# Kernel tuning notes

Measured on AMD Instinct MI355X. Metric: run time of the kernel, lower is better.

The kernel has to match this reference:

```python
import jax, jax.numpy as jnp
import numpy as np

B, S, H = 2, 2048, 2048
NH, NKV, D = 16, 8, 128
THETA = 10000.0
EPS = 1e-6
SCALE = D ** -0.5


def setup_inputs() -> dict:
    key = jax.random.key(0)
    k0, k1, k2 = jax.random.split(key, 3)
    hidden_states = jax.random.normal(k0, (B, S, H), dtype=jnp.float32)
    position_ids = jnp.arange(B * S, dtype=jnp.int64).reshape(B, S) % S
    w_qkv = jax.random.normal(k1, (NH * D + 2 * NKV * D, H), dtype=jnp.float32) * 0.02
    w_o = jax.random.normal(k2, (H, NH * D), dtype=jnp.float32) * 0.02
    q_norm_w = jnp.ones((D,), dtype=jnp.float32)
    k_norm_w = jnp.ones((D,), dtype=jnp.float32)
    return {"hidden_states": hidden_states, "position_ids": position_ids,
            "w_qkv": w_qkv, "w_o": w_o, "q_norm_w": q_norm_w, "k_norm_w": k_norm_w}


def _rms_norm(x, w):
    # x: [..., D]; vLLM RMSNorm: x * rsqrt(mean(x^2) + eps) * w
    var = jnp.mean(x * x, axis=-1, keepdims=True)
    return x * jax.lax.rsqrt(var + EPS) * w


def _rope_gptj(x, positions):
    # non-neox (GPT-J interleaved) RoPE. x: [B, S, nheads, D], positions: [B, S]
    inv_freq = 1.0 / (THETA ** (jnp.arange(0, D, 2, dtype=jnp.float32) / D))  # [D/2]
    freqs = positions.astype(jnp.float32)[..., None] * inv_freq  # [B, S, D/2]
    cos = jnp.repeat(jnp.cos(freqs), 2, axis=-1)[:, :, None, :]  # [B, S, 1, D]
    sin = jnp.repeat(jnp.sin(freqs), 2, axis=-1)[:, :, None, :]
    x1 = x[..., ::2]
    x2 = x[..., 1::2]
    rot = jnp.stack([-x2, x1], axis=-1).reshape(x.shape)  # interleaved rotate
    return x * cos + rot * sin


def reference(hidden_states, position_ids, w_qkv, w_o, q_norm_w, k_norm_w):
    bsz, seq_len, _ = hidden_states.shape
    qkv = jnp.einsum('bsh,oh->bso', hidden_states, w_qkv)  # [B, S, q+2kv]
    q, k, v = jnp.split(qkv, [NH * D, NH * D + NKV * D], axis=-1)
    q = q.reshape(bsz, seq_len, NH, D)
    k = k.reshape(bsz, seq_len, NKV, D)
    v = v.reshape(bsz, seq_len, NKV, D)
    q = _rms_norm(q, q_norm_w)
    k = _rms_norm(k, k_norm_w)
    q = _rope_gptj(q, position_ids)
    k = _rope_gptj(k, position_ids)
    # GQA: group q heads over kv heads
    G = NH // NKV
    qg = q.reshape(bsz, seq_len, NKV, G, D)
    # scores: [B, NKV, G, S, S]
    scores = jnp.einsum('bqhgd,bkhd->bhgqk', qg, k) * SCALE
    causal = jnp.tril(jnp.ones((seq_len, seq_len), dtype=bool))
    scores = jnp.where(causal, scores, jnp.float32(-1e30))
    probs = jax.nn.softmax(scores, axis=-1)
    out = jnp.einsum('bhgqk,bkhd->bqhgd', probs, v)  # [B, S, NKV, G, D]
    out = out.reshape(bsz, seq_len, NH * D)
    return jnp.einsum('bsd,hd->bsh', out, w_o)  # [B, S, H]
```

## Files before the change

### kernel.cpp

```cpp
#include <hip/hip_runtime.h>
#include <hip/hip_bf16.h>
#include <cstdint>
#include <cstddef>


typedef __attribute__((ext_vector_type(8))) short bf16x8;
typedef __attribute__((ext_vector_type(4))) float f32x4;

#define B_ 2
#define S_ 2048
#define H_ 2048
#define NH_ 16
#define NKV_ 8
#define D_ 128
#define BS_ 4096
#define QKVO_ 4096

__device__ __forceinline__ unsigned short f2bf(float f) {
  union { float f; unsigned u; } v; v.f = f;
  unsigned u = v.u;
  u += 0x7fffu + ((u >> 16) & 1u);
  return (unsigned short)(u >> 16);
}

__device__ __forceinline__ void gload_lds16(const void* g, void* l) {
  __builtin_amdgcn_global_load_lds(
      (const __attribute__((address_space(1))) unsigned int*)g,
      (__attribute__((address_space(3))) unsigned int*)l, 16, 0, 0);
}

__global__ void k_f32_to_bf16(const float* __restrict__ x,
                              unsigned short* __restrict__ y, int n4) {
  int i = blockIdx.x * blockDim.x + threadIdx.x;
  if (i >= n4) return;
  float4 v = ((const float4*)x)[i];
  ushort4 o;
  o.x = f2bf(v.x); o.y = f2bf(v.y); o.z = f2bf(v.z); o.w = f2bf(v.w);
  ((ushort4*)y)[i] = o;
}

#define BM 128
#define BN 128
#define BK 32

__global__ __launch_bounds__(256, 2) void k_gemm_bf16(
    const unsigned short* __restrict__ A, const unsigned short* __restrict__ Bm,
    float* __restrict__ C, int M, int N, int K) {
  __shared__ __align__(16) char lds[2][2][BM * BK * 2];

  int nwg = gridDim.x;
  int bid = blockIdx.x;
  int cpx = nwg >> 3;
  int swz = (bid & 7) * cpx + (bid >> 3);
  int nbn = N / BN;
  int bm = swz / nbn, bn = swz % nbn;

  int tid = threadIdx.x;
  int lane = tid & 63, w = tid >> 6;
  int wr = w >> 1, wc = w & 1;
  int lq = lane & 15, lk = lane >> 4;

  const unsigned short* Abase = A + (size_t)bm * BM * K;
  const unsigned short* Bbase = Bm + (size_t)bn * BN * K;

  f32x4 acc[4][4] = {};
  int nt = K / BK;

  auto stage = [&](int buf, int t) {
#pragma unroll
    for (int j = 0; j < 2; ++j) {
      int s = (tid + j * 256) * 16;
      int row = s >> 6;
      int cb = s & 48;
      int cs = cb ^ (((row >> 1) & 3) << 4);
      const char* ga = (const char*)(Abase + (size_t)row * K + t * BK) + cs;
      const char* gb = (const char*)(Bbase + (size_t)row * K + t * BK) + cs;
      gload_lds16(ga, &lds[buf][0][s]);
      gload_lds16(gb, &lds[buf][1][s]);
    }
  };

  stage(0, 0);
  __syncthreads();

  int cur = 0;
  for (int t = 0; t < nt; ++t) {
    if (t + 1 < nt) stage(cur ^ 1, t + 1);
    bf16x8 af[4], bfr[4];
#pragma unroll
    for (int m = 0; m < 4; ++m) {
      int row = wr * 64 + m * 16 + lq;
      int addr = row * 64 + ((lk * 16) ^ (((row >> 1) & 3) << 4));
      af[m] = *(const bf16x8*)(&lds[cur][0][addr]);
    }
#pragma unroll
    for (int n = 0; n < 4; ++n) {
      int row = wc * 64 + n * 16 + lq;
      int addr = row * 64 + ((lk * 16) ^ (((row >> 1) & 3) << 4));
      bfr[n] = *(const bf16x8*)(&lds[cur][1][addr]);
    }
#pragma unroll
    for (int m = 0; m < 4; ++m)
#pragma unroll
      for (int n = 0; n < 4; ++n)
        acc[m][n] = __builtin_amdgcn_mfma_f32_16x16x32_bf16(af[m], bfr[n], acc[m][n], 0, 0, 0);
    __syncthreads();
    cur ^= 1;
  }

#pragma unroll
  for (int m = 0; m < 4; ++m) {
    int row0 = bm * BM + wr * 64 + m * 16 + lk * 4;
#pragma unroll
    for (int n = 0; n < 4; ++n) {
      int col = bn * BN + wc * 64 + n * 16 + lq;
#pragma unroll
      for (int r = 0; r < 4; ++r)
        C[(size_t)(row0 + r) * N + col] = acc[m][n][r];
    }
  }
}

__global__ void k_norm_rope(const float* __restrict__ qkv,
                            const int* __restrict__ pos,
                            const float* __restrict__ qw,
                            const float* __restrict__ kw,
                            unsigned short* __restrict__ Qb,
                            unsigned short* __restrict__ Kb) {
  int g = blockIdx.x * 4 + (threadIdx.x >> 6);
  int lane = threadIdx.x & 63;
  int t = g / 24;
  int slot = g % 24;
  bool isq = slot < 16;
  int h = isq ? slot : slot - 16;
  int off = isq ? h * D_ : NH_ * D_ + h * D_;
  const float* w = isq ? qw : kw;

  float2 x = *(const float2*)(qkv + (size_t)t * QKVO_ + off + lane * 2);
  float ss = x.x * x.x + x.y * x.y;
#pragma unroll
  for (int o = 1; o < 64; o <<= 1) ss += __shfl_xor(ss, o);
  float inv = rsqrtf(ss * (1.0f / 128.0f) + 1e-6f);
  float2 wv = *(const float2*)(w + lane * 2);
  float x1 = x.x * inv * wv.x;
  float x2 = x.y * inv * wv.y;

  float p = (float)pos[t];
  float invf = exp2f(-(float)(lane * 2) * (13.287712379549449f / 128.0f));
  float ang = p * invf;
  float sn, cs;
  sincosf(ang, &sn, &cs);
  float y1 = x1 * cs - x2 * sn;
  float y2 = x2 * cs + x1 * sn;

  int b = t >> 11;
  int sq = t & (S_ - 1);
  size_t o_;
  unsigned short* dst;
  if (isq) { o_ = (((size_t)b * NH_ + h) * S_ + sq) * D_ + lane * 2; dst = Qb; }
  else     { o_ = (((size_t)b * NKV_ + h) * S_ + sq) * D_ + lane * 2; dst = Kb; }
  ushort2 ov; ov.x = f2bf(y1); ov.y = f2bf(y2);
  *(ushort2*)(dst + o_) = ov;
}

__global__ void k_v_transpose(const float* __restrict__ qkv,
                              unsigned short* __restrict__ Vt) {
  __shared__ unsigned short tile[128][72];
  int bidx = blockIdx.x;
  int st = bidx & 31;
  int kh = (bidx >> 5) & 7;
  int b = bidx >> 8;
  int s0 = st * 64;
  int tid = threadIdx.x;
#pragma unroll
  for (int i = 0; i < 8; ++i) {
    int idx = tid + i * 256;
    int row = idx >> 5, c4 = idx & 31;
    float4 v = *(const float4*)(qkv + ((size_t)(b * S_ + s0 + row)) * QKVO_ +
                                (NH_ + NKV_) * D_ + kh * D_ + c4 * 4);
    tile[c4 * 4 + 0][row] = f2bf(v.x);
    tile[c4 * 4 + 1][row] = f2bf(v.y);
    tile[c4 * 4 + 2][row] = f2bf(v.z);
    tile[c4 * 4 + 3][row] = f2bf(v.w);
  }
  __syncthreads();
#pragma unroll
  for (int i = 0; i < 8; ++i) {
    int idx = tid + i * 256;
    int d = idx >> 4, c4 = idx & 15;
    ushort4 o;
    o.x = tile[d][c4 * 4 + 0]; o.y = tile[d][c4 * 4 + 1];
    o.z = tile[d][c4 * 4 + 2]; o.w = tile[d][c4 * 4 + 3];
    *(ushort4*)(Vt + ((((size_t)b * NKV_ + kh) * D_ + d) * S_) + s0 + c4 * 4) = o;
  }
}

#define QBLK 128
#define KVB 64

__global__ __launch_bounds__(256, 2) void k_attn(
    const unsigned short* __restrict__ Qb, const unsigned short* __restrict__ Kb,
    const unsigned short* __restrict__ Vt, unsigned short* __restrict__ Ob) {
  __shared__ __align__(16) char Ks[2][KVB * D_ * 2];
  __shared__ __align__(16) char Vs[2][D_ * KVB * 2];
  __shared__ __align__(16) char Ps[4][32 * KVB * 2];

  int x = blockIdx.x;
  int u = x & 255;
  int hi = x >> 8;
  int k_ = u & 15;
  int qt = hi ? k_ : 15 - k_;
  int h = u >> 4;
  int b = hi;
  int kvh = h >> 1;
  int q0 = qt * QBLK;
  int tid = threadIdx.x, lane = tid & 63, w = tid >> 6;
  int lq = lane & 15, lk = lane >> 4;

  const unsigned short* Qhead = Qb + ((size_t)b * NH_ + h) * S_ * D_;
  const unsigned short* Khead = Kb + ((size_t)b * NKV_ + kvh) * S_ * D_;
  const unsigned short* Vthead = Vt + ((size_t)b * NKV_ + kvh) * D_ * S_;

  bf16x8 qf[2][4];
#pragma unroll
  for (int m = 0; m < 2; ++m)
#pragma unroll
    for (int ks = 0; ks < 4; ++ks)
      qf[m][ks] = *(const bf16x8*)(Qhead +
          (size_t)(q0 + w * 32 + m * 16 + lq) * D_ + ks * 32 + lk * 8);

  f32x4 o_acc[2][8] = {};
  float mrow[2][4], lrow[2][4];
#pragma unroll
  for (int m = 0; m < 2; ++m)
#pragma unroll
    for (int r = 0; r < 4; ++r) { mrow[m][r] = -1e30f; lrow[m][r] = 0.0f; }

  int ntile = q0 / KVB + 2;

  auto stageKV = [&](int buf, int t) {
    int kv0 = t * KVB;
#pragma unroll
    for (int j = 0; j < 4; ++j) {
      int s = (tid + j * 256) * 16;
      {
        int row = s >> 8, cb = s & 255;
        int cs = cb ^ ((row & 7) << 4);
        const char* g = (const char*)(Khead + (size_t)(kv0 + row) * D_) + cs;
        gload_lds16(g, &Ks[buf][s]);
      }
      {
        int row = s >> 7, cb = s & 127;
        int cs = cb ^ ((row & 7) << 4);
        const char* g = (const char*)(Vthead + (size_t)row * S_ + kv0) + cs;
        gload_lds16(g, &Vs[buf][s]);
      }
    }
  };

  stageKV(0, 0);
  __syncthreads();

  const float c1 = 0.08838834764831845f * 1.4426950408889634f;

  int cur = 0;
  for (int t = 0; t < ntile; ++t) {
    if (t + 1 < ntile) stageKV(cur ^ 1, t + 1);
    int kv0 = t * KVB;

    f32x4 sc[2][4] = {};
#pragma unroll
    for (int ks = 0; ks < 4; ++ks) {
      bf16x8 kf[4];
#pragma unroll
      for (int n = 0; n < 4; ++n) {
        int row = n * 16 + lq;
        int addr = row * 256 + ((ks * 64 + lk * 16) ^ ((row & 7) << 4));
        kf[n] = *(const bf16x8*)(&Ks[cur][addr]);
      }
#pragma unroll
      for (int m = 0; m < 2; ++m)
#pragma unroll
        for (int n = 0; n < 4; ++n)
          sc[m][n] = __builtin_amdgcn_mfma_f32_16x16x32_bf16(qf[m][ks], kf[n], sc[m][n], 0, 0, 0);
    }

    bool diag = (kv0 + KVB > q0);
#pragma unroll
    for (int m = 0; m < 2; ++m) {
      float pm[4][4];
      float corr[4];
#pragma unroll
      for (int r = 0; r < 4; ++r) {
        int qg = q0 + w * 32 + m * 16 + lk * 4 + r;
        float vmax = -1e30f;
        float sv[4];
#pragma unroll
        for (int n = 0; n < 4; ++n) {
          float xv = sc[m][n][r] * c1;
          if (diag && (kv0 + n * 16 + lq > qg)) xv = -1e30f;
          sv[n] = xv;
          vmax = fmaxf(vmax, xv);
        }
#pragma unroll
        for (int o = 1; o < 16; o <<= 1) vmax = fmaxf(vmax, __shfl_xor(vmax, o));
        float mnew = fmaxf(mrow[m][r], vmax);
        float cr = exp2f(mrow[m][r] - mnew);
        mrow[m][r] = mnew;
        float rs = 0.0f;
#pragma unroll
        for (int n = 0; n < 4; ++n) {
          float pv = exp2f(sv[n] - mnew);
          pm[n][r] = pv;
          rs += pv;
        }
#pragma unroll
        for (int o = 1; o < 16; o <<= 1) rs += __shfl_xor(rs, o);
        lrow[m][r] = lrow[m][r] * cr + rs;
        corr[r] = cr;
      }
#pragma unroll
      for (int nd = 0; nd < 8; ++nd)
#pragma unroll
        for (int r = 0; r < 4; ++r) o_acc[m][nd][r] *= corr[r];
#pragma unroll
      for (int n = 0; n < 4; ++n)
#pragma unroll
        for (int r = 0; r < 4; ++r) {
          int qlocal = m * 16 + lk * 4 + r;
          int kb = (n * 16 + lq) * 2;
          int addr = qlocal * 128 + (kb ^ ((qlocal & 7) << 4));
          *(unsigned short*)(&Ps[w][addr]) = f2bf(pm[n][r]);
        }
    }

#pragma unroll
    for (int ks = 0; ks < 2; ++ks) {
      bf16x8 pa[2];
#pragma unroll
      for (int m = 0; m < 2; ++m) {
        int row = m * 16 + lq;
        int addr = row * 128 + ((ks * 64 + lk * 16) ^ ((row & 7) << 4));
        pa[m] = *(const bf16x8*)(&Ps[w][addr]);
      }
#pragma unroll
      for (int nd = 0; nd < 8; ++nd) {
        int row = nd * 16 + lq;
        int addr = row * 128 + ((ks * 64 + lk * 16) ^ ((row & 7) << 4));
        bf16x8 vf = *(const bf16x8*)(&Vs[cur][addr]);
#pragma unroll
        for (int m = 0; m < 2; ++m)
          o_acc[m][nd] = __builtin_amdgcn_mfma_f32_16x16x32_bf16(pa[m], vf, o_acc[m][nd], 0, 0, 0);
      }
    }
    __syncthreads();
    cur ^= 1;
  }

#pragma unroll
  for (int m = 0; m < 2; ++m)
#pragma unroll
    for (int r = 0; r < 4; ++r) {
      float rl = 1.0f / lrow[m][r];
      int qg = q0 + w * 32 + m * 16 + lk * 4 + r;
      size_t base = ((size_t)b * S_ + qg) * (NH_ * D_) + h * D_;
#pragma unroll
      for (int nd = 0; nd < 8; ++nd)
        Ob[base + nd * 16 + lq] = f2bf(o_acc[m][nd][r] * rl);
    }
}

extern "C" void kernel_launch(void* const* d_in, const int* in_sizes, int n_in,
                              void* d_out, int out_size, void* d_ws, size_t ws_size,
                              hipStream_t stream) {
  const float* hs    = (const float*)d_in[0];
  const int*   pos   = (const int*)d_in[1];
  const float* w_qkv = (const float*)d_in[2];
  const float* w_o   = (const float*)d_in[3];
  const float* qw    = (const float*)d_in[4];
  const float* kw    = (const float*)d_in[5];
  float* out = (float*)d_out;

  char* ws = (char*)d_ws;
  unsigned short* Xbf  = (unsigned short*)ws;
  unsigned short* Wqbf = Xbf + (size_t)BS_ * H_;
  unsigned short* Wobf = Wqbf + (size_t)QKVO_ * H_;
  float* qkv = (float*)(Wobf + (size_t)H_ * (NH_ * D_));
  unsigned short* Qb  = (unsigned short*)(qkv + (size_t)BS_ * QKVO_);
  unsigned short* Kb  = Qb + (size_t)B_ * NH_ * S_ * D_;
  unsigned short* Vtb = Kb + (size_t)B_ * NKV_ * S_ * D_;
  unsigned short* Ab  = Vtb + (size_t)B_ * NKV_ * S_ * D_;

  k_f32_to_bf16<<<(BS_ * H_ / 4) / 256, 256, 0, stream>>>(hs, Xbf, BS_ * H_ / 4);
  k_f32_to_bf16<<<(QKVO_ * H_ / 4) / 256, 256, 0, stream>>>(w_qkv, Wqbf, QKVO_ * H_ / 4);
  k_f32_to_bf16<<<(H_ * NH_ * D_ / 4) / 256, 256, 0, stream>>>(w_o, Wobf, H_ * NH_ * D_ / 4);

  k_gemm_bf16<<<(BS_ / BM) * (QKVO_ / BN), 256, 0, stream>>>(
      Xbf, Wqbf, qkv, BS_, QKVO_, H_);

  k_norm_rope<<<BS_ * 24 / 4, 256, 0, stream>>>(qkv, pos, qw, kw, Qb, Kb);

  k_v_transpose<<<B_ * NKV_ * (S_ / 64), 256, 0, stream>>>(qkv, Vtb);

  k_attn<<<(S_ / QBLK) * NH_ * B_, 256, 0, stream>>>(Qb, Kb, Vtb, Ab);

  k_gemm_bf16<<<(BS_ / BM) * (H_ / BN), 256, 0, stream>>>(
      Ab, Wobf, out, BS_, H_, H_);
}
```

Baseline: 416.8 us.

## Pair causal query strips per 512-thread block and transpose score MFMA layout

Each attention block now has 8 waves and handles two 128-row query strips, one with a light causal load and one with a heavy one, so work is balanced within a block and only 256 blocks are launched. The waves share K/V staging in LDS, and waves whose strip has finished skip compute while still joining the barriers. The score MFMA operands are swapped so each lane holds one query row, which makes the softmax reductions cheaper (two shuffles instead of four). P is packed with the hardware bf16 pack instruction, and s_setprio is raised around the MFMA sections. In exchange, the light-strip waves sit idle for part of the loop, and the larger blocks may reduce occupancy.

```diff
diff --git a/kernel.cpp b/kernel.cpp
--- a/kernel.cpp
+++ b/kernel.cpp
@@ -21,6 +21,12 @@
   unsigned u = v.u;
   u += 0x7fffu + ((u >> 16) & 1u);
   return (unsigned short)(u >> 16);
+}
+
+__device__ __forceinline__ unsigned cvt_pk_bf16(float lo, float hi) {
+  unsigned r;
+  asm("v_cvt_pk_bf16_f32 %0, %1, %2" : "=v"(r) : "v"(lo), "v"(hi));
+  return r;
 }
 
 __device__ __forceinline__ void gload_lds16(const void* g, void* l) {
@@ -195,27 +201,28 @@
   }
 }
 
-#define QBLK 128
 #define KVB 64
 
-__global__ __launch_bounds__(256, 2) void k_attn(
+__global__ __launch_bounds__(512, 2) void k_attn(
     const unsigned short* __restrict__ Qb, const unsigned short* __restrict__ Kb,
     const unsigned short* __restrict__ Vt, unsigned short* __restrict__ Ob) {
   __shared__ __align__(16) char Ks[2][KVB * D_ * 2];
   __shared__ __align__(16) char Vs[2][D_ * KVB * 2];
-  __shared__ __align__(16) char Ps[4][32 * KVB * 2];
+  __shared__ __align__(16) char Ps[8][32 * KVB * 2];
 
   int x = blockIdx.x;
-  int u = x & 255;
-  int hi = x >> 8;
-  int k_ = u & 15;
-  int qt = hi ? k_ : 15 - k_;
-  int h = u >> 4;
-  int b = hi;
+  int kk = x >> 5;
+  int bh = x & 31;
+  int b = bh >> 4, h = bh & 15;
   int kvh = h >> 1;
-  int q0 = qt * QBLK;
+
   int tid = threadIdx.x, lane = tid & 63, w = tid >> 6;
   int lq = lane & 15, lk = lane >> 4;
+  int strip = w >> 2, wq = w & 3;
+  int qt = strip ? kk : 15 - kk;
+  int q0w = qt * 128 + wq * 32;
+  int nt_w = ((q0w + 31) >> 6) + 1;
+  int nt_max = 2 * (15 - kk) + 2;
 
   const unsigned short* Qhead = Qb + ((size_t)b * NH_ + h) * S_ * D_;
   const unsigned short* Khead = Kb + ((size_t)b * NKV_ + kvh) * S_ * D_;
@@ -227,22 +234,17 @@
 #pragma unroll
     for (int ks = 0; ks < 4; ++ks)
       qf[m][ks] = *(const bf16x8*)(Qhead +
-          (size_t)(q0 + w * 32 + m * 16 + lq) * D_ + ks * 32 + lk * 8);
+          (size_t)(q0w + m * 16 + lq) * D_ + ks * 32 + lk * 8);
 
   f32x4 o_acc[2][8] = {};
-  float mrow[2][4], lrow[2][4];
-#pragma unroll
-  for (int m = 0; m < 2; ++m)
-#pragma unroll
-    for (int r = 0; r < 4; ++r) { mrow[m][r] = -1e30f; lrow[m][r] = 0.0f; }
-
-  int ntile = q0 / KVB + 2;
+  float mrow[2] = {-1e30f, -1e30f};
+  float lrow[2] = {0.0f, 0.0f};
 
   auto stageKV = [&](int buf, int t) {
     int kv0 = t * KVB;
 #pragma unroll
-    for (int j = 0; j < 4; ++j) {
-      int s = (tid + j * 256) * 16;
+    for (int j = 0; j < 2; ++j) {
+      int s = (tid + j * 512) * 16;
       {
         int row = s >> 8, cb = s & 255;
         int cs = cb ^ ((row & 7) << 4);
@@ -250,9 +252,9 @@
         gload_lds16(g, &Ks[buf][s]);
       }
       {
-        int row = s >> 7, cb = s & 127;
-        int cs = cb ^ ((row & 7) << 4);
-        const char* g = (const char*)(Vthead + (size_t)row * S_ + kv0) + cs;
+        int rv = s >> 7, cv = s & 127;
+        int cs = cv ^ ((rv & 7) << 4);
+        const char* g = (const char*)(Vthead + (size_t)rv * S_ + kv0) + cs;
         gload_lds16(g, &Vs[buf][s]);
       }
     }
@@ -264,94 +266,103 @@
   const float c1 = 0.08838834764831845f * 1.4426950408889634f;
 
   int cur = 0;
-  for (int t = 0; t < ntile; ++t) {
-    if (t + 1 < ntile) stageKV(cur ^ 1, t + 1);
-    int kv0 = t * KVB;
-
-    f32x4 sc[2][4] = {};
-#pragma unroll
-    for (int ks = 0; ks < 4; ++ks) {
-      bf16x8 kf[4];
-#pragma unroll
-      for (int n = 0; n < 4; ++n) {
-        int row = n * 16 + lq;
-        int addr = row * 256 + ((ks * 64 + lk * 16) ^ ((row & 7) << 4));
-        kf[n] = *(const bf16x8*)(&Ks[cur][addr]);
+  for (int t = 0; t < nt_max; ++t) {
+    if (t + 1 < nt_max) stageKV(cur ^ 1, t + 1);
+    if (t < nt_w) {
+      int kv0 = t * KVB;
+
+      f32x4 sc[4][2] = {};
+      __builtin_amdgcn_s_setprio(1);
+#pragma unroll
+      for (int ks = 0; ks < 4; ++ks) {
+        bf16x8 kf[4];
+#pragma unroll
+        for (int n = 0; n < 4; ++n) {
+          int row = n * 16 + lq;
+          int addr = row * 256 + ((ks * 64 + lk * 16) ^ ((row & 7) << 4));
+          kf[n] = *(const bf16x8*)(&Ks[cur][addr]);
+        }
+#pragma unroll
+        for (int n = 0; n < 4; ++n)
+#pragma unroll
+          for (int m = 0; m < 2; ++m)
+            sc[n][m] = __builtin_amdgcn_mfma_f32_16x16x32_bf16(kf[n], qf[m][ks], sc[n][m], 0, 0, 0);
       }
-#pragma unroll
-      for (int m = 0; m < 2; ++m)
+      __builtin_amdgcn_s_setprio(0);
+
+      bool diag = (kv0 + KVB > q0w);
+#pragma unroll
+      for (int m = 0; m < 2; ++m) {
+        int qg = q0w + m * 16 + lq;
+        float sv[4][4];
+        float vmax = -1e30f;
 #pragma unroll
         for (int n = 0; n < 4; ++n)
-          sc[m][n] = __builtin_amdgcn_mfma_f32_16x16x32_bf16(qf[m][ks], kf[n], sc[m][n], 0, 0, 0);
-    }
-
-    bool diag = (kv0 + KVB > q0);
-#pragma unroll
-    for (int m = 0; m < 2; ++m) {
-      float pm[4][4];
-      float corr[4];
-#pragma unroll
-      for (int r = 0; r < 4; ++r) {
-        int qg = q0 + w * 32 + m * 16 + lk * 4 + r;
-        float vmax = -1e30f;
-        float sv[4];
+#pragma unroll
+          for (int r = 0; r < 4; ++r) {
+            float xv = sc[n][m][r] * c1;
+            if (diag && (kv0 + n * 16 + lk * 4 + r > qg)) xv = -1e30f;
+            sv[n][r] = xv;
+            vmax = fmaxf(vmax, xv);
+          }
+        vmax = fmaxf(vmax, __shfl_xor(vmax, 16));
+        vmax = fmaxf(vmax, __shfl_xor(vmax, 32));
+        float mnew = fmaxf(mrow[m], vmax);
+        float cr = exp2f(mrow[m] - mnew);
+        mrow[m] = mnew;
+        float rs = 0.0f;
+#pragma unroll
+        for (int n = 0; n < 4; ++n)
+#pragma unroll
+          for (int r = 0; r < 4; ++r) {
+            float pv = exp2f(sv[n][r] - mnew);
+            sv[n][r] = pv;
+            rs += pv;
+          }
+        rs += __shfl_xor(rs, 16);
+        rs += __shfl_xor(rs, 32);
+        lrow[m] = lrow[m] * cr + rs;
+
+        float crr[4];
+#pragma unroll
+        for (int r = 0; r < 4; ++r) crr[r] = __shfl(cr, lk * 4 + r);
+#pragma unroll
+        for (int nd = 0; nd < 8; ++nd)
+#pragma unroll
+          for (int r = 0; r < 4; ++r) o_acc[m][nd][r] *= crr[r];
+
+        int qlocal = m * 16 + lq;
 #pragma unroll
         for (int n = 0; n < 4; ++n) {
-          float xv = sc[m][n][r] * c1;
-          if (diag && (kv0 + n * 16 + lq > qg)) xv = -1e30f;
-          sv[n] = xv;
-          vmax = fmaxf(vmax, xv);
+          uint2 pk_;
+          pk_.x = cvt_pk_bf16(sv[n][0], sv[n][1]);
+          pk_.y = cvt_pk_bf16(sv[n][2], sv[n][3]);
+          int addr = qlocal * 128 + ((n * 32 + lk * 8) ^ ((qlocal & 7) << 4));
+          *(uint2*)(&Ps[w][addr]) = pk_;
         }
-#pragma unroll
-        for (int o = 1; o < 16; o <<= 1) vmax = fmaxf(vmax, __shfl_xor(vmax, o));
-        float mnew = fmaxf(mrow[m][r], vmax);
-        float cr = exp2f(mrow[m][r] - mnew);
-        mrow[m][r] = mnew;
-        float rs = 0.0f;
-#pragma unroll
-        for (int n = 0; n < 4; ++n) {
-          float pv = exp2f(sv[n] - mnew);
-          pm[n][r] = pv;
-          rs += pv;
+      }
+
+      __builtin_amdgcn_s_setprio(1);
+#pragma unroll
+      for (int ks = 0; ks < 2; ++ks) {
+        bf16x8 pa[2];
+#pragma unroll
+        for (int m = 0; m < 2; ++m) {
+          int row = m * 16 + lq;
+          int addr = row * 128 + ((ks * 64 + lk * 16) ^ ((row & 7) << 4));
+          pa[m] = *(const bf16x8*)(&Ps[w][addr]);
         }
 #pragma unroll
-        for (int o = 1; o < 16; o <<= 1) rs += __shfl_xor(rs, o);
-        lrow[m][r] = lrow[m][r] * cr + rs;
-        corr[r] = cr;
+        for (int nd = 0; nd < 8; ++nd) {
+          int row = nd * 16 + lq;
+          int addr = row * 128 + ((ks * 64 + lk * 16) ^ ((row & 7) << 4));
+          bf16x8 vf = *(const bf16x8*)(&Vs[cur][addr]);
+#pragma unroll
+          for (int m = 0; m < 2; ++m)
+            o_acc[m][nd] = __builtin_amdgcn_mfma_f32_16x16x32_bf16(pa[m], vf, o_acc[m][nd], 0, 0, 0);
+        }
       }
-#pragma unroll
-      for (int nd = 0; nd < 8; ++nd)
-#pragma unroll
-        for (int r = 0; r < 4; ++r) o_acc[m][nd][r] *= corr[r];
-#pragma unroll
-      for (int n = 0; n < 4; ++n)
-#pragma unroll
-        for (int r = 0; r < 4; ++r) {
-          int qlocal = m * 16 + lk * 4 + r;
-          int kb = (n * 16 + lq) * 2;
-          int addr = qlocal * 128 + (kb ^ ((qlocal & 7) << 4));
-          *(unsigned short*)(&Ps[w][addr]) = f2bf(pm[n][r]);
-        }
-    }
-
-#pragma unroll
-    for (int ks = 0; ks < 2; ++ks) {
-      bf16x8 pa[2];
-#pragma unroll
-      for (int m = 0; m < 2; ++m) {
-        int row = m * 16 + lq;
-        int addr = row * 128 + ((ks * 64 + lk * 16) ^ ((row & 7) << 4));
-        pa[m] = *(const bf16x8*)(&Ps[w][addr]);
-      }
-#pragma unroll
-      for (int nd = 0; nd < 8; ++nd) {
-        int row = nd * 16 + lq;
-        int addr = row * 128 + ((ks * 64 + lk * 16) ^ ((row & 7) << 4));
-        bf16x8 vf = *(const bf16x8*)(&Vs[cur][addr]);
-#pragma unroll
-        for (int m = 0; m < 2; ++m)
-          o_acc[m][nd] = __builtin_amdgcn_mfma_f32_16x16x32_bf16(pa[m], vf, o_acc[m][nd], 0, 0, 0);
-      }
+      __builtin_amdgcn_s_setprio(0);
     }
     __syncthreads();
     cur ^= 1;
@@ -361,8 +372,9 @@
   for (int m = 0; m < 2; ++m)
 #pragma unroll
     for (int r = 0; r < 4; ++r) {
-      float rl = 1.0f / lrow[m][r];
-      int qg = q0 + w * 32 + m * 16 + lk * 4 + r;
+      float lv = __shfl(lrow[m], lk * 4 + r);
+      float rl = 1.0f / lv;
+      int qg = q0w + m * 16 + lk * 4 + r;
       size_t base = ((size_t)b * S_ + qg) * (NH_ * D_) + h * D_;
 #pragma unroll
       for (int nd = 0; nd < 8; ++nd)
@@ -402,7 +414,7 @@
 
   k_v_transpose<<<B_ * NKV_ * (S_ / 64), 256, 0, stream>>>(qkv, Vtb);
 
-  k_attn<<<(S_ / QBLK) * NH_ * B_, 256, 0, stream>>>(Qb, Kb, Vtb, Ab);
+  k_attn<<<256, 512, 0, stream>>>(Qb, Kb, Vtb, Ab);
 
   k_gemm_bf16<<<(BS_ / BM) * (H_ / BN), 256, 0, stream>>>(
       Ab, Wobf, out, BS_, H_, H_);
```

Result: faster. 377.6 us (-9.4%).
